# Optimization experiments

Measured on AMD Instinct MI355X. Metric: run time of the kernel, lower is better.

The kernel has to match this reference:

```python
import jax, jax.numpy as jnp
import numpy as np
from jax import lax

B, T, H, L, NV = 2048, 100, 256, 128, 5  # batch, max_len, hidden, latent, len(NUC_VOCAB)


def setup_inputs() -> dict:
    key = jax.random.key(0)
    ks = jax.random.split(key, 13)
    s = 0.05
    inp = {
        "x_seq": jax.random.uniform(ks[0], (B, T, NV), dtype=jnp.float32),
        "hidden_states": jax.random.normal(ks[1], (B, H), dtype=jnp.float32) * 0.1,
        "tree_latent_vec": jax.random.normal(ks[2], (B, L), dtype=jnp.float32),
        "graph_latent_vec": jax.random.normal(ks[3], (B, L), dtype=jnp.float32),
        "lengths": jnp.maximum(1, jax.random.randint(ks[4], (B,), 0, T + 1)).astype(jnp.int32),
        # concat_squash_linear: (H + L) -> H
        "W_cs": jax.random.normal(ks[5], (H + L, H), dtype=jnp.float32) * s,
        "b_cs": jnp.zeros((H,), dtype=jnp.float32),
        # GRU cell linears: (H + NV) -> H, acting on cat([x, h])
        "W_z": jax.random.normal(ks[6], (NV + H, H), dtype=jnp.float32) * s,
        "b_z": jnp.zeros((H,), dtype=jnp.float32),
        "W_r": jax.random.normal(ks[7], (NV + H, H), dtype=jnp.float32) * s,
        "b_r": jnp.zeros((H,), dtype=jnp.float32),
        "W_h": jax.random.normal(ks[8], (NV + H, H), dtype=jnp.float32) * s,
        "b_h": jnp.zeros((H,), dtype=jnp.float32),
    }
    return inp


def _decode(x_seq, hidden_states, tree_latent_vec, graph_latent_vec, lengths,
            W_cs, b_cs, W_z, b_z, W_r, b_r, W_h, b_h):
    # concat volatile hidden state with graph latent, squash back to H
    h0 = jax.nn.relu(jnp.concatenate([hidden_states, graph_latent_vec], axis=-1) @ W_cs + b_cs)

    def gru_step(h, x):  # h: [B,H], x: [B,NV]
        xh = jnp.concatenate([x, h], axis=-1)          # [B, NV+H]
        z = jax.nn.sigmoid(xh @ W_z + b_z)
        r = jax.nn.sigmoid(xh @ W_r + b_r)
        xg = jnp.concatenate([x, r * h], axis=-1)
        pre_h = jnp.tanh(xg @ W_h + b_h)
        new_h = (1.0 - z) * h + z * pre_h
        return new_h, new_h

    _, hs = lax.scan(gru_step, h0, jnp.swapaxes(x_seq, 0, 1))  # [T,B,H]
    all_h = jnp.swapaxes(hs, 0, 1)                              # [B,T,H]

    # gather hidden state at last valid timestep (pre_padding_idx)
    new_h = jnp.take_along_axis(all_h, (lengths - 1)[:, None, None], axis=1)[:, 0]  # [B,H]

    # per-segment max-pool over valid positions (segment_representation)
    mask = jnp.arange(T)[None, :] < lengths[:, None]            # [B,T]
    seg_rep = jnp.max(jnp.where(mask[:, :, None], all_h, -jnp.inf), axis=1)  # [B,H]

    # depadded token features concatenated with per-batch tree/graph latents;
    # kept padded [B,T,.] with zeros at invalid positions (fixed-shape form)
    tok = jnp.concatenate([
        all_h,
        jnp.broadcast_to(tree_latent_vec[:, None, :], (B, T, L)),
        jnp.broadcast_to(graph_latent_vec[:, None, :], (B, T, L)),
    ], axis=-1)                                                 # [B,T,H+2L]
    all_hidden_states = jnp.where(mask[:, :, None], tok, 0.0)
    return new_h, all_hidden_states, seg_rep


def reference(x_seq, hidden_states, tree_latent_vec, graph_latent_vec, lengths,
              W_cs, b_cs, W_z, b_z, W_r, b_r, W_h, b_h):
    return _decode(x_seq, hidden_states, tree_latent_vec, graph_latent_vec, lengths,
                   W_cs, b_cs, W_z, b_z, W_r, b_r, W_h, b_h)
```

## Files before the change

### kernel.cpp

```cpp
#include <hip/hip_runtime.h>
#include <stdint.h>

#define B_N 2048
#define T_N 100
#define H_N 256
#define L_N 128
#define NV_N 5
#define COLS 512

#define KCS 384
#define RB 8

#define KT_N 9
#define PZ_STR 260
#define HB_STR 296

#define NKQ 2
#define KQH 128
#define CH 16
#define NCH 8
#define HSTR 264

static constexpr int OUT_ALLH = B_N * H_N;
static constexpr int OUT_SEG  = OUT_ALLH + B_N * T_N * COLS;

typedef __attribute__((ext_vector_type(8))) short bf16x8v;
typedef __attribute__((ext_vector_type(4))) float f32x4v;

__device__ __align__(16) uint16_t g_frag[3 * KT_N * 16 * 64 * 8];

__device__ __forceinline__ float bits2f(uint32_t u) {
    union { uint32_t u; float f; } v; v.u = u; return v.f;
}
__device__ __forceinline__ uint16_t f2bf(float f) {
    union { float f; uint32_t u; } v; v.f = f;
    uint32_t r = (v.u + 0x7FFFu + ((v.u >> 16) & 1u)) >> 16;
    return (uint16_t)r;
}

__device__ __forceinline__ int detect_f32(const uint32_t* __restrict__ w) {
    int cnt = 0;
    #pragma unroll 8
    for (int i = 0; i < 64; ++i) {
        uint32_t e = (w[i] >> 23) & 0xFFu;
        cnt += (e >= 97u && e <= 130u) ? 1 : 0;
    }
    return cnt >= 32 ? 1 : 0;
}

__device__ __forceinline__ float bld1(const void* p, int idx) {
    return bits2f(((uint32_t)((const uint16_t*)p)[idx]) << 16);
}
__device__ __forceinline__ void bld4(const void* p, int idx, float f[4]) {
    uint2 u = *(const uint2*)((const uint16_t*)p + idx);
    f[0] = bits2f(u.x << 16); f[1] = bits2f(u.x & 0xFFFF0000u);
    f[2] = bits2f(u.y << 16); f[3] = bits2f(u.y & 0xFFFF0000u);
}
__device__ __forceinline__ void bst4(void* p, int idx, const float f[4]) {
    uint2 u;
    u.x = (uint32_t)f2bf(f[0]) | ((uint32_t)f2bf(f[1]) << 16);
    u.y = (uint32_t)f2bf(f[2]) | ((uint32_t)f2bf(f[3]) << 16);
    *(uint2*)((uint16_t*)p + idx) = u;
}
__device__ __forceinline__ void bst4z(void* p, int idx) {
    *(uint2*)((uint16_t*)p + idx) = make_uint2(0u, 0u);
}

template <bool F32> struct IO;
template <> struct IO<true> {
    using Raw2 = float2;
    static __device__ __forceinline__ Raw2 ldraw2(const void* p, int idx) {
        return *(const float2*)((const float*)p + idx);
    }
    static __device__ __forceinline__ void cvt2(const Raw2& u, float f[2]) { f[0] = u.x; f[1] = u.y; }
    static __device__ __forceinline__ void ld4(const void* p, int idx, float f[4]) {
        const float4 v = *(const float4*)((const float*)p + idx);
        f[0] = v.x; f[1] = v.y; f[2] = v.z; f[3] = v.w;
    }
    static __device__ __forceinline__ float ld1(const void* p, int idx) { return ((const float*)p)[idx]; }
    static __device__ __forceinline__ void st4(void* p, int idx, const float f[4]) {
        *(float4*)((float*)p + idx) = make_float4(f[0], f[1], f[2], f[3]);
    }
    static __device__ __forceinline__ void st4z(void* p, int idx) {
        *(float4*)((float*)p + idx) = make_float4(0.f, 0.f, 0.f, 0.f);
    }
};
template <> struct IO<false> {
    using Raw2 = uint32_t;
    static __device__ __forceinline__ Raw2 ldraw2(const void* p, int idx) {
        return *(const uint32_t*)((const uint16_t*)p + idx);
    }
    static __device__ __forceinline__ void cvt2(const Raw2& u, float f[2]) {
        f[0] = bits2f(u << 16); f[1] = bits2f(u & 0xFFFF0000u);
    }
    static __device__ __forceinline__ void ld4(const void* p, int idx, float f[4]) { bld4(p, idx, f); }
    static __device__ __forceinline__ float ld1(const void* p, int idx) { return bld1(p, idx); }
    static __device__ __forceinline__ void st4(void* p, int idx, const float f[4]) { bst4(p, idx, f); }
    static __device__ __forceinline__ void st4z(void* p, int idx) { bst4z(p, idx); }
};

__device__ __forceinline__ float sigmoid_f(float x) {
    x = fminf(fmaxf(x, -30.f), 30.f);
    return 1.f / (1.f + __expf(-x));
}
__device__ __forceinline__ float tanh_f(float x) {
    x = fminf(fmaxf(x, -15.f), 15.f);
    float e = __expf(-2.f * x);
    return (1.f - e) / (1.f + e);
}

template <bool F32>
__global__ __launch_bounds__(256) void latent_fill_kernel(
    const void* __restrict__ tree,
    const void* __restrict__ graph,
    const int* __restrict__ lengths,
    const void* __restrict__ Wcs_detect,
    void* __restrict__ out)
{
    __shared__ int s_is32;
    if (threadIdx.x == 0) s_is32 = detect_f32((const uint32_t*)Wcs_detect);
    __syncthreads();
    if ((s_is32 != 0) != F32) return;

    int idx = (int)(blockIdx.x * 256 + threadIdx.x);
    int c = (idx & 31) * 8;
    int bt = idx >> 5;
    int t = bt % T_N;
    int b = bt / T_N;

    int dst = OUT_ALLH + bt * COLS + H_N + c;
    if (t < lengths[b]) {
        float v[8];
        if (c < L_N) {
            IO<F32>::ld4(tree, b * L_N + c, v);
            IO<F32>::ld4(tree, b * L_N + c + 4, v + 4);
        } else {
            IO<F32>::ld4(graph, b * L_N + (c - L_N), v);
            IO<F32>::ld4(graph, b * L_N + (c - L_N) + 4, v + 4);
        }
        IO<F32>::st4(out, dst, v);
        IO<F32>::st4(out, dst + 4, v + 4);
    } else {
        IO<F32>::st4z(out, dst);
        IO<F32>::st4z(out, dst + 4);
    }
}

__global__ __launch_bounds__(256) void prep_kernel(
    const void* __restrict__ Wz, const void* __restrict__ Wr,
    const void* __restrict__ Wh, const void* __restrict__ Wcs_detect)
{
    __shared__ int s_is32;
    if (threadIdx.x == 0) s_is32 = detect_f32((const uint32_t*)Wcs_detect);
    __syncthreads();
    const int is32 = s_is32;

    int g = (int)(blockIdx.x * 256 + threadIdx.x);
    int lane  = g & 63;
    int rest  = g >> 6;
    int nt    = rest & 15;
    int rest2 = rest >> 4;
    int kt    = rest2 % KT_N;
    int mat   = rest2 / KT_N;
    if (mat > 2) return;

    const void* W = (mat == 0) ? Wz : (mat == 1) ? Wr : Wh;
    const int n = nt * 16 + (lane & 15);
    uint16_t u[8];
    #pragma unroll
    for (int j = 0; j < 8; ++j) {
        int k = kt * 32 + ((lane >> 4) * 8) + j;
        int srow = (k < 256) ? (k + NV_N) : ((k <= 260) ? (k - 256) : -1);
        uint16_t v = 0;
        if (srow >= 0) {
            if (is32) v = f2bf(((const float*)W)[srow * H_N + n]);
            else      v = ((const uint16_t*)W)[srow * H_N + n];
        }
        u[j] = v;
    }
    uint4 o;
    o.x = (uint32_t)u[0] | ((uint32_t)u[1] << 16);
    o.y = (uint32_t)u[2] | ((uint32_t)u[3] << 16);
    o.z = (uint32_t)u[4] | ((uint32_t)u[5] << 16);
    o.w = (uint32_t)u[6] | ((uint32_t)u[7] << 16);
    *(uint4*)((char*)g_frag + (size_t)g * 16) = o;
}

__global__ __launch_bounds__(256, 1) void gru_mfma(
    const void* __restrict__ x_seq,
    const void* __restrict__ hidden,
    const void* __restrict__ graph,
    const int* __restrict__ lengths,
    const void* __restrict__ Wcs, const void* __restrict__ bcs,
    const void* __restrict__ bz,  const void* __restrict__ br,
    const void* __restrict__ bh,  void* __restrict__ out)
{
    __shared__ float PzS[16 * PZ_STR];
    __shared__ float PrS[16 * PZ_STR];
    __shared__ uint16_t hbf[16 * HB_STR];
    __shared__ uint16_t gbf[16 * HB_STR];
    __shared__ int s_is32;
    __shared__ int s_len[RB];

    if (threadIdx.x == 0) s_is32 = detect_f32((const uint32_t*)Wcs);
    __syncthreads();
    if (s_is32 != 0) return;

    const int tid  = threadIdx.x;
    const int lane = tid & 63;
    const int wv   = tid >> 6;
    const int ntb  = wv * 4;
    const int ro   = tid >> 5;
    const int c0g  = (tid & 31) * 8;

    if (tid < RB) {
        int L = lengths[blockIdx.x * RB + tid];
        s_len[tid] = min(max(L, 1), T_N);
    }
    for (int i = tid; i < 16 * HB_STR; i += 256) { hbf[i] = 0; gbf[i] = 0; }
    __syncthreads();

    const int b0  = blockIdx.x * RB;
    const int bo  = b0 + ro;
    const int len = s_len[ro];
    int maxlen = 1;
    #pragma unroll
    for (int i = 0; i < RB; ++i) maxlen = max(maxlen, s_len[i]);

    {
        float* cs = PzS;
        for (int i = tid; i < RB * KCS; i += 256) {
            int r = i / KCS, k = i - r * KCS;
            int bb = b0 + r;
            float v = (k < H_N) ? bld1(hidden, bb * H_N + k)
                                : bld1(graph,  bb * L_N + (k - H_N));
            cs[r * 388 + k] = v;
        }
    }
    __syncthreads();

    float h[8];
    {
        const float* cs = PzS;
        float acc[8];
        bld4(bcs, c0g, acc); bld4(bcs, c0g + 4, acc + 4);
        for (int k = 0; k < KCS; k += 4) {
            const float4 hv = *(const float4*)&cs[ro * 388 + k];
            const float hvv[4] = {hv.x, hv.y, hv.z, hv.w};
            #pragma unroll
            for (int kk = 0; kk < 4; ++kk) {
                float w[8];
                bld4(Wcs, (k + kk) * H_N + c0g, w);
                bld4(Wcs, (k + kk) * H_N + c0g + 4, w + 4);
                #pragma unroll
                for (int j = 0; j < 8; ++j) acc[j] += hvv[kk] * w[j];
            }
        }
        #pragma unroll
        for (int j = 0; j < 8; ++j) h[j] = fmaxf(acc[j], 0.f);
    }

    float bzv[8], brv[8], bhv[8];
    bld4(bz, c0g, bzv); bld4(bz, c0g + 4, bzv + 4);
    bld4(br, c0g, brv); bld4(br, c0g + 4, brv + 4);
    bld4(bh, c0g, bhv); bld4(bh, c0g + 4, bhv + 4);

    float smax[8];
    #pragma unroll
    for (int j = 0; j < 8; ++j) smax[j] = -1e30f;

    __syncthreads();

#define STORE_HILO(BUF, VALS) { \
    union { bf16x8v v; uint16_t u[8]; } hi_, lo_; \
    _Pragma("unroll") \
    for (int j_ = 0; j_ < 8; ++j_) { \
        uint16_t a_ = f2bf(VALS[j_]); \
        hi_.u[j_] = a_; \
        lo_.u[j_] = f2bf(VALS[j_] - bits2f((uint32_t)a_ << 16)); \
    } \
    *(bf16x8v*)&BUF[ro * HB_STR + c0g] = hi_.v; \
    *(bf16x8v*)&BUF[(8 + ro) * HB_STR + c0g] = lo_.v; }

    STORE_HILO(hbf, h)
    const int xr = tid / NV_N;
    const int xi = tid - xr * NV_N;
    float xv = 0.f;
    if (tid < RB * NV_N) {
        float x0 = bld1(x_seq, ((b0 + xr) * T_N + 0) * NV_N + xi);
        uint16_t xh = f2bf(x0);
        uint16_t xl = f2bf(x0 - bits2f((uint32_t)xh << 16));
        hbf[xr * HB_STR + 256 + xi] = xh; hbf[(8 + xr) * HB_STR + 256 + xi] = xl;
        gbf[xr * HB_STR + 256 + xi] = xh; gbf[(8 + xr) * HB_STR + 256 + xi] = xl;
        xv = bld1(x_seq, ((b0 + xr) * T_N + 1) * NV_N + xi);
    }
    __syncthreads();

    const bf16x8v* wsW = (const bf16x8v*)g_frag;
    float z[8];

#define LDB1(KT, S) { \
    _Pragma("unroll") \
    for (int nt_ = 0; nt_ < 4; ++nt_) { \
        Bz[S][nt_] = wsW[((0 * KT_N + (KT)) * 16 + ntb + nt_) * 64 + lane]; \
        Br[S][nt_] = wsW[((1 * KT_N + (KT)) * 16 + ntb + nt_) * 64 + lane]; \
    } }
#define MMA1(KT, S) { \
    bf16x8v a_ = *(const bf16x8v*)&hbf[(lane & 15) * HB_STR + (KT) * 32 + ((lane >> 4) * 8)]; \
    _Pragma("unroll") \
    for (int nt_ = 0; nt_ < 4; ++nt_) { \
        accz[nt_] = __builtin_amdgcn_mfma_f32_16x16x32_bf16(a_, Bz[S][nt_], accz[nt_], 0, 0, 0); \
        accr[nt_] = __builtin_amdgcn_mfma_f32_16x16x32_bf16(a_, Br[S][nt_], accr[nt_], 0, 0, 0); \
    } }
#define LDB2(KT, S) { \
    _Pragma("unroll") \
    for (int nt_ = 0; nt_ < 4; ++nt_) \
        Bh[S][nt_] = wsW[((2 * KT_N + (KT)) * 16 + ntb + nt_) * 64 + lane]; }
#define MMA2(KT, S) { \
    bf16x8v a_ = *(const bf16x8v*)&gbf[(lane & 15) * HB_STR + (KT) * 32 + ((lane >> 4) * 8)]; \
    _Pragma("unroll") \
    for (int nt_ = 0; nt_ < 4; ++nt_) \
        acch[nt_] = __builtin_amdgcn_mfma_f32_16x16x32_bf16(a_, Bh[S][nt_], acch[nt_], 0, 0, 0); }

    #pragma unroll 1
    for (int t = 0; t < maxlen; ++t) {
        {
            bf16x8v Bz[3][4], Br[3][4];
            f32x4v accz[4], accr[4];
            #pragma unroll
            for (int nt_ = 0; nt_ < 4; ++nt_) {
                accz[nt_] = {0.f, 0.f, 0.f, 0.f};
                accr[nt_] = {0.f, 0.f, 0.f, 0.f};
            }
            LDB1(0, 0) LDB1(1, 1) LDB1(2, 2)
            MMA1(0, 0) LDB1(3, 0)
            MMA1(1, 1) LDB1(4, 1)
            MMA1(2, 2) LDB1(5, 2)
            MMA1(3, 0) LDB1(6, 0)
            MMA1(4, 1) LDB1(7, 1)
            MMA1(5, 2) LDB1(8, 2)
            MMA1(6, 0) MMA1(7, 1) MMA1(8, 2)
            #pragma unroll
            for (int nt_ = 0; nt_ < 4; ++nt_) {
                #pragma unroll
                for (int i_ = 0; i_ < 4; ++i_) {
                    const int m_ = (lane >> 4) * 4 + i_;
                    const int cc = (ntb + nt_) * 16 + (lane & 15);
                    PzS[m_ * PZ_STR + cc] = accz[nt_][i_];
                    PrS[m_ * PZ_STR + cc] = accr[nt_][i_];
                }
            }
        }
        __syncthreads();

        {
            const float4 za = *(const float4*)&PzS[ro * PZ_STR + c0g];
            const float4 zb = *(const float4*)&PzS[ro * PZ_STR + c0g + 4];
            const float4 zc = *(const float4*)&PzS[(8 + ro) * PZ_STR + c0g];
            const float4 zd = *(const float4*)&PzS[(8 + ro) * PZ_STR + c0g + 4];
            const float4 ra = *(const float4*)&PrS[ro * PZ_STR + c0g];
            const float4 rb = *(const float4*)&PrS[ro * PZ_STR + c0g + 4];
            const float4 rc = *(const float4*)&PrS[(8 + ro) * PZ_STR + c0g];
            const float4 rd = *(const float4*)&PrS[(8 + ro) * PZ_STR + c0g + 4];
            float sz[8] = {bzv[0] + za.x + zc.x, bzv[1] + za.y + zc.y,
                           bzv[2] + za.z + zc.z, bzv[3] + za.w + zc.w,
                           bzv[4] + zb.x + zd.x, bzv[5] + zb.y + zd.y,
                           bzv[6] + zb.z + zd.z, bzv[7] + zb.w + zd.w};
            float sr[8] = {brv[0] + ra.x + rc.x, brv[1] + ra.y + rc.y,
                           brv[2] + ra.z + rc.z, brv[3] + ra.w + rc.w,
                           brv[4] + rb.x + rd.x, brv[5] + rb.y + rd.y,
                           brv[6] + rb.z + rd.z, brv[7] + rb.w + rd.w};
            float rh[8];
            #pragma unroll
            for (int j = 0; j < 8; ++j) {
                z[j]  = sigmoid_f(sz[j]);
                rh[j] = sigmoid_f(sr[j]) * h[j];
            }
            STORE_HILO(gbf, rh)
        }
        __syncthreads();

        {
            bf16x8v Bh[3][4];
            f32x4v acch[4];
            #pragma unroll
            for (int nt_ = 0; nt_ < 4; ++nt_) acch[nt_] = {0.f, 0.f, 0.f, 0.f};
            LDB2(0, 0) LDB2(1, 1) LDB2(2, 2)
            MMA2(0, 0) LDB2(3, 0)
            MMA2(1, 1) LDB2(4, 1)
            MMA2(2, 2) LDB2(5, 2)
            MMA2(3, 0) LDB2(6, 0)
            MMA2(4, 1) LDB2(7, 1)
            MMA2(5, 2) LDB2(8, 2)
            MMA2(6, 0) MMA2(7, 1) MMA2(8, 2)
            #pragma unroll
            for (int nt_ = 0; nt_ < 4; ++nt_) {
                #pragma unroll
                for (int i_ = 0; i_ < 4; ++i_) {
                    const int m_ = (lane >> 4) * 4 + i_;
                    PzS[m_ * PZ_STR + (ntb + nt_) * 16 + (lane & 15)] = acch[nt_][i_];
                }
            }
        }
        __syncthreads();

        {
            const float4 ga = *(const float4*)&PzS[ro * PZ_STR + c0g];
            const float4 gb = *(const float4*)&PzS[ro * PZ_STR + c0g + 4];
            const float4 gc = *(const float4*)&PzS[(8 + ro) * PZ_STR + c0g];
            const float4 gd = *(const float4*)&PzS[(8 + ro) * PZ_STR + c0g + 4];
            float sg[8] = {bhv[0] + ga.x + gc.x, bhv[1] + ga.y + gc.y,
                           bhv[2] + ga.z + gc.z, bhv[3] + ga.w + gc.w,
                           bhv[4] + gb.x + gd.x, bhv[5] + gb.y + gd.y,
                           bhv[6] + gb.z + gd.z, bhv[7] + gb.w + gd.w};
            const bool active = (t < len);
            float hs[8];
            #pragma unroll
            for (int j = 0; j < 8; ++j) {
                float pre = tanh_f(sg[j]);
                float hn  = (1.f - z[j]) * h[j] + z[j] * pre;
                hn = active ? hn : h[j];
                h[j]  = hn;
                hs[j] = active ? hn : 0.f;
                smax[j] = active ? fmaxf(smax[j], hn) : smax[j];
            }
            const int ob = OUT_ALLH + (bo * T_N + t) * COLS + c0g;
            bst4(out, ob, hs);
            bst4(out, ob + 4, hs + 4);
            if (t == len - 1) {
                bst4(out, bo * H_N + c0g, h);
                bst4(out, bo * H_N + c0g + 4, h + 4);
            }
            STORE_HILO(hbf, h)
        }
        if (tid < RB * NV_N) {
            uint16_t xh = f2bf(xv);
            uint16_t xl = f2bf(xv - bits2f((uint32_t)xh << 16));
            hbf[xr * HB_STR + 256 + xi] = xh; hbf[(8 + xr) * HB_STR + 256 + xi] = xl;
            gbf[xr * HB_STR + 256 + xi] = xh; gbf[(8 + xr) * HB_STR + 256 + xi] = xl;
            int tn = (t + 2 < T_N) ? (t + 2) : (T_N - 1);
            xv = bld1(x_seq, ((b0 + xr) * T_N + tn) * NV_N + xi);
        }
        __syncthreads();
    }

#undef LDB1
#undef MMA1
#undef LDB2
#undef MMA2
#undef STORE_HILO

    for (int t = maxlen; t < T_N; ++t) {
        const int ob = OUT_ALLH + (bo * T_N + t) * COLS + c0g;
        bst4z(out, ob);
        bst4z(out, ob + 4);
    }
    bst4(out, OUT_SEG + bo * H_N + c0g, smax);
    bst4(out, OUT_SEG + bo * H_N + c0g + 4, smax + 4);
}

template <bool F32>
__global__ __launch_bounds__(256, 1) void gru_kernel(
    const void* __restrict__ x_seq,
    const void* __restrict__ hidden,
    const void* __restrict__ graph,
    const int* __restrict__ lengths,
    const void* __restrict__ Wcs, const void* __restrict__ bcs,
    const void* __restrict__ Wz,  const void* __restrict__ bz,
    const void* __restrict__ Wr,  const void* __restrict__ br,
    const void* __restrict__ Wh,  const void* __restrict__ bh,
    void* __restrict__ out)
{
    __shared__ float Pz[NKQ][RB][H_N];
    __shared__ float Pr[NKQ][RB][H_N];
    __shared__ float hstage[RB][HSTR];
    __shared__ float gstage[RB][HSTR];
    __shared__ int s_is32;
    __shared__ int s_len[RB];

    if (threadIdx.x == 0) s_is32 = detect_f32((const uint32_t*)Wcs);
    __syncthreads();
    if ((s_is32 != 0) != F32) return;

    const int tid = threadIdx.x;
    const int kq  = tid >> 7;
    const int c0  = (tid & 127) * 2;
    const int ro  = tid >> 5;
    const int c0g = (tid & 31) * 8;
    const int kh0 = kq * KQH;

    if (tid < RB) {
        int L = lengths[blockIdx.x * RB + tid];
        s_len[tid] = min(max(L, 1), T_N);
    }
    __syncthreads();

    const int b0  = blockIdx.x * RB;
    const int bo  = b0 + ro;
    const int len = s_len[ro];
    int maxlen = 1;
    #pragma unroll
    for (int i = 0; i < RB; ++i) maxlen = max(maxlen, s_len[i]);

    {
        float* cs = &Pz[0][0][0];
        for (int i = tid; i < RB * KCS; i += 256) {
            int r = i / KCS;
            int k = i - r * KCS;
            int bb = b0 + r;
            float v = (k < H_N) ? IO<F32>::ld1(hidden, bb * H_N + k)
                                : IO<F32>::ld1(graph,  bb * L_N + (k - H_N));
            cs[r * 388 + k] = v;
        }
    }
    __syncthreads();

    float h[8];
    {
        const float* cs = &Pz[0][0][0];
        float acc[8];
        IO<F32>::ld4(bcs, c0g, acc);
        IO<F32>::ld4(bcs, c0g + 4, acc + 4);
        for (int k = 0; k < KCS; k += 4) {
            const float4 hv = *reinterpret_cast<const float4*>(&cs[ro * 388 + k]);
            const float hvv[4] = {hv.x, hv.y, hv.z, hv.w};
            #pragma unroll
            for (int kk = 0; kk < 4; ++kk) {
                float w[8];
                IO<F32>::ld4(Wcs, (k + kk) * H_N + c0g, w);
                IO<F32>::ld4(Wcs, (k + kk) * H_N + c0g + 4, w + 4);
                #pragma unroll
                for (int j = 0; j < 8; ++j) acc[j] += hvv[kk] * w[j];
            }
        }
        #pragma unroll
        for (int j = 0; j < 8; ++j) h[j] = fmaxf(acc[j], 0.f);
    }

    float bzv[8], brv[8], bhv[8];
    IO<F32>::ld4(bz, c0g, bzv); IO<F32>::ld4(bz, c0g + 4, bzv + 4);
    IO<F32>::ld4(br, c0g, brv); IO<F32>::ld4(br, c0g + 4, brv + 4);
    IO<F32>::ld4(bh, c0g, bhv); IO<F32>::ld4(bh, c0g + 4, bhv + 4);

    float smax[8];
    #pragma unroll
    for (int j = 0; j < 8; ++j) smax[j] = -1e30f;

    __syncthreads();

    *reinterpret_cast<float4*>(&hstage[ro][c0g])     = make_float4(h[0], h[1], h[2], h[3]);
    *reinterpret_cast<float4*>(&hstage[ro][c0g + 4]) = make_float4(h[4], h[5], h[6], h[7]);

    const int xr = tid / NV_N;
    const int xi = tid - xr * NV_N;
    float xv = 0.f;
    if (tid < RB * NV_N) {
        float x0 = IO<F32>::ld1(x_seq, ((b0 + xr) * T_N + 0) * NV_N + xi);
        hstage[xr][H_N + xi] = x0;
        gstage[xr][H_N + xi] = x0;
        int tn = (1 < T_N) ? 1 : 0;
        xv = IO<F32>::ld1(x_seq, ((b0 + xr) * T_N + tn) * NV_N + xi);
    }
    __syncthreads();

    float z[8];
    typename IO<F32>::Raw2 zA[CH], rA[CH], zB[CH], rB[CH], hA[CH], hB[CH];
    typename IO<F32>::Raw2 xzb[NV_N], xrb[NV_N], xhb[NV_N];

#define P1_ISSUE(CHN, RZ, RR) { \
    const int kb_ = 5 + kh0 + (CHN) * CH; \
    _Pragma("unroll") \
    for (int i_ = 0; i_ < CH; ++i_) { \
        RZ[i_] = IO<F32>::ldraw2(Wz, (kb_ + i_) * H_N + c0); \
        RR[i_] = IO<F32>::ldraw2(Wr, (kb_ + i_) * H_N + c0); \
    } \
    __builtin_amdgcn_sched_barrier(0); }
#define P1_CONSUME(CHN, RZ, RR) { \
    const int kb_ = kh0 + (CHN) * CH; \
    _Pragma("unroll") \
    for (int g_ = 0; g_ < CH / 2; ++g_) { \
        float2 hr_[RB]; \
        _Pragma("unroll") \
        for (int r_ = 0; r_ < RB; ++r_) \
            hr_[r_] = *reinterpret_cast<const float2*>(&hstage[r_][kb_ + 2 * g_]); \
        _Pragma("unroll") \
        for (int u_ = 0; u_ < 2; ++u_) { \
            float wz2_[2], wr2_[2]; \
            IO<F32>::cvt2(RZ[2 * g_ + u_], wz2_); \
            IO<F32>::cvt2(RR[2 * g_ + u_], wr2_); \
            _Pragma("unroll") \
            for (int r_ = 0; r_ < RB; ++r_) { \
                const float hv_ = u_ ? hr_[r_].y : hr_[r_].x; \
                az[r_][0] += hv_ * wz2_[0]; \
                az[r_][1] += hv_ * wz2_[1]; \
                ar[r_][0] += hv_ * wr2_[0]; \
                ar[r_][1] += hv_ * wr2_[1]; \
            } } } }
#define P2_ISSUE(CHN, RH) { \
    const int kb_ = 5 + kh0 + (CHN) * CH; \
    _Pragma("unroll") \
    for (int i_ = 0; i_ < CH; ++i_) \
        RH[i_] = IO<F32>::ldraw2(Wh, (kb_ + i_) * H_N + c0); \
    __builtin_amdgcn_sched_barrier(0); }
#define P2_CONSUME(CHN, RH) { \
    const int kb_ = kh0 + (CHN) * CH; \
    _Pragma("unroll") \
    for (int g_ = 0; g_ < CH / 2; ++g_) { \
        float2 gr_[RB]; \
        _Pragma("unroll") \
        for (int r_ = 0; r_ < RB; ++r_) \
            gr_[r_] = *reinterpret_cast<const float2*>(&gstage[r_][kb_ + 2 * g_]); \
        _Pragma("unroll") \
        for (int u_ = 0; u_ < 2; ++u_) { \
            float wh2_[2]; \
            IO<F32>::cvt2(RH[2 * g_ + u_], wh2_); \
            _Pragma("unroll") \
            for (int r_ = 0; r_ < RB; ++r_) { \
                const float gv_ = u_ ? gr_[r_].y : gr_[r_].x; \
                ag[r_][0] += gv_ * wh2_[0]; \
                ag[r_][1] += gv_ * wh2_[1]; \
            } } } }
#define PX_ISSUE() if (kq == 0) { \
    _Pragma("unroll") \
    for (int i_ = 0; i_ < NV_N; ++i_) { \
        xzb[i_] = IO<F32>::ldraw2(Wz, i_ * H_N + c0); \
        xrb[i_] = IO<F32>::ldraw2(Wr, i_ * H_N + c0); \
    } }
#define PXH_ISSUE() if (kq == 0) { \
    _Pragma("unroll") \
    for (int i_ = 0; i_ < NV_N; ++i_) \
        xhb[i_] = IO<F32>::ldraw2(Wh, i_ * H_N + c0); }
#define P1X_CONSUME() if (kq == 0) { \
    _Pragma("unroll") \
    for (int i_ = 0; i_ < NV_N; ++i_) { \
        float wz2_[2], wr2_[2]; \
        IO<F32>::cvt2(xzb[i_], wz2_); \
        IO<F32>::cvt2(xrb[i_], wr2_); \
        _Pragma("unroll") \
        for (int r_ = 0; r_ < RB; ++r_) { \
            const float xv_ = hstage[r_][H_N + i_]; \
            az[r_][0] += xv_ * wz2_[0]; \
            az[r_][1] += xv_ * wz2_[1]; \
            ar[r_][0] += xv_ * wr2_[0]; \
            ar[r_][1] += xv_ * wr2_[1]; \
        } } }
#define P2X_CONSUME() if (kq == 0) { \
    _Pragma("unroll") \
    for (int i_ = 0; i_ < NV_N; ++i_) { \
        float wh2_[2]; \
        IO<F32>::cvt2(xhb[i_], wh2_); \
        _Pragma("unroll") \
        for (int r_ = 0; r_ < RB; ++r_) { \
            const float xv_ = gstage[r_][H_N + i_]; \
            ag[r_][0] += xv_ * wh2_[0]; \
            ag[r_][1] += xv_ * wh2_[1]; \
        } } }

    PX_ISSUE();
    P1_ISSUE(0, zA, rA);

    #pragma unroll 1
    for (int t = 0; t < maxlen; ++t) {
        float az[RB][2], ar[RB][2];
        #pragma unroll
        for (int r = 0; r < RB; ++r) {
            az[r][0] = 0.f; az[r][1] = 0.f;
            ar[r][0] = 0.f; ar[r][1] = 0.f;
        }
        #pragma unroll 1
        for (int ch = 0; ch < NCH; ch += 2) {
            P1_ISSUE(ch + 1, zB, rB);
            P1_CONSUME(ch, zA, rA);
            if (ch + 2 < NCH) { P1_ISSUE(ch + 2, zA, rA); }
            else              { P2_ISSUE(0, hA); PXH_ISSUE(); }
            P1_CONSUME(ch + 1, zB, rB);
        }
        P1X_CONSUME();
        #pragma unroll
        for (int r = 0; r < RB; ++r) {
            *reinterpret_cast<float2*>(&Pz[kq][r][c0]) = make_float2(az[r][0], az[r][1]);
            *reinterpret_cast<float2*>(&Pr[kq][r][c0]) = make_float2(ar[r][0], ar[r][1]);
        }
        __syncthreads();

        {
            float sz[8], sr[8];
            #pragma unroll
            for (int j = 0; j < 8; ++j) { sz[j] = bzv[j]; sr[j] = brv[j]; }
            #pragma unroll
            for (int q = 0; q < NKQ; ++q) {
                float4 a = *reinterpret_cast<const float4*>(&Pz[q][ro][c0g]);
                float4 b = *reinterpret_cast<const float4*>(&Pz[q][ro][c0g + 4]);
                sz[0] += a.x; sz[1] += a.y; sz[2] += a.z; sz[3] += a.w;
                sz[4] += b.x; sz[5] += b.y; sz[6] += b.z; sz[7] += b.w;
                a = *reinterpret_cast<const float4*>(&Pr[q][ro][c0g]);
                b = *reinterpret_cast<const float4*>(&Pr[q][ro][c0g + 4]);
                sr[0] += a.x; sr[1] += a.y; sr[2] += a.z; sr[3] += a.w;
                sr[4] += b.x; sr[5] += b.y; sr[6] += b.z; sr[7] += b.w;
            }
            float rh[8];
            #pragma unroll
            for (int j = 0; j < 8; ++j) {
                z[j] = sigmoid_f(sz[j]);
                rh[j] = sigmoid_f(sr[j]) * h[j];
            }
            *reinterpret_cast<float4*>(&gstage[ro][c0g])     = make_float4(rh[0], rh[1], rh[2], rh[3]);
            *reinterpret_cast<float4*>(&gstage[ro][c0g + 4]) = make_float4(rh[4], rh[5], rh[6], rh[7]);
        }
        __syncthreads();

        float ag[RB][2];
        #pragma unroll
        for (int r = 0; r < RB; ++r) { ag[r][0] = 0.f; ag[r][1] = 0.f; }
        #pragma unroll 1
        for (int ch = 0; ch < NCH; ch += 2) {
            P2_ISSUE(ch + 1, hB);
            P2_CONSUME(ch, hA);
            if (ch + 2 < NCH) { P2_ISSUE(ch + 2, hA); }
            else              { P1_ISSUE(0, zA, rA); PX_ISSUE(); }
            P2_CONSUME(ch + 1, hB);
        }
        P2X_CONSUME();
        #pragma unroll
        for (int r = 0; r < RB; ++r)
            *reinterpret_cast<float2*>(&Pz[kq][r][c0]) = make_float2(ag[r][0], ag[r][1]);
        __syncthreads();

        {
            float sg[8];
            #pragma unroll
            for (int j = 0; j < 8; ++j) sg[j] = bhv[j];
            #pragma unroll
            for (int q = 0; q < NKQ; ++q) {
                float4 a = *reinterpret_cast<const float4*>(&Pz[q][ro][c0g]);
                float4 b = *reinterpret_cast<const float4*>(&Pz[q][ro][c0g + 4]);
                sg[0] += a.x; sg[1] += a.y; sg[2] += a.z; sg[3] += a.w;
                sg[4] += b.x; sg[5] += b.y; sg[6] += b.z; sg[7] += b.w;
            }
            const bool active = (t < len);
            float hs[8];
            #pragma unroll
            for (int j = 0; j < 8; ++j) {
                float pre = tanh_f(sg[j]);
                float hn  = (1.f - z[j]) * h[j] + z[j] * pre;
                hn = active ? hn : h[j];
                h[j]  = hn;
                hs[j] = active ? hn : 0.f;
                smax[j] = active ? fmaxf(smax[j], hn) : smax[j];
            }
            const int ob = OUT_ALLH + (bo * T_N + t) * COLS + c0g;
            IO<F32>::st4(out, ob, hs);
            IO<F32>::st4(out, ob + 4, hs + 4);
            if (t == len - 1) {
                IO<F32>::st4(out, bo * H_N + c0g, h);
                IO<F32>::st4(out, bo * H_N + c0g + 4, h + 4);
            }
            *reinterpret_cast<float4*>(&hstage[ro][c0g])     = make_float4(h[0], h[1], h[2], h[3]);
            *reinterpret_cast<float4*>(&hstage[ro][c0g + 4]) = make_float4(h[4], h[5], h[6], h[7]);
        }
        if (tid < RB * NV_N) {
            hstage[xr][H_N + xi] = xv;
            gstage[xr][H_N + xi] = xv;
            int tn = (t + 2 < T_N) ? (t + 2) : (T_N - 1);
            xv = IO<F32>::ld1(x_seq, ((b0 + xr) * T_N + tn) * NV_N + xi);
        }
        __syncthreads();
    }

#undef P1_ISSUE
#undef P1_CONSUME
#undef P2_ISSUE
#undef P2_CONSUME
#undef PX_ISSUE
#undef PXH_ISSUE
#undef P1X_CONSUME
#undef P2X_CONSUME

    for (int t = maxlen; t < T_N; ++t) {
        const int ob = OUT_ALLH + (bo * T_N + t) * COLS + c0g;
        IO<F32>::st4z(out, ob);
        IO<F32>::st4z(out, ob + 4);
    }
    IO<F32>::st4(out, OUT_SEG + bo * H_N + c0g, smax);
    IO<F32>::st4(out, OUT_SEG + bo * H_N + c0g + 4, smax + 4);
}

extern "C" void kernel_launch(void* const* d_in, const int* in_sizes, int n_in,
                              void* d_out, int out_size, void* d_ws, size_t ws_size,
                              hipStream_t stream) {
    const void* x_seq  = d_in[0];
    const void* hidden = d_in[1];
    const void* tree   = d_in[2];
    const void* graph  = d_in[3];
    const int*  lens   = (const int*)d_in[4];
    const void* Wcs    = d_in[5];
    const void* bcs    = d_in[6];
    const void* Wz     = d_in[7];
    const void* bz     = d_in[8];
    const void* Wr     = d_in[9];
    const void* br     = d_in[10];
    const void* Wh     = d_in[11];
    const void* bh     = d_in[12];
    void* out = d_out;
    (void)d_ws; (void)ws_size;

    long long work = (long long)B_N * T_N * 32;
    int fill_blocks = (int)(work / 256);

    hipLaunchKernelGGL((latent_fill_kernel<true>),  dim3(fill_blocks), dim3(256), 0, stream,
                       tree, graph, lens, Wcs, out);
    hipLaunchKernelGGL((latent_fill_kernel<false>), dim3(fill_blocks), dim3(256), 0, stream,
                       tree, graph, lens, Wcs, out);

    hipLaunchKernelGGL(prep_kernel, dim3(108), dim3(256), 0, stream,
                       Wz, Wr, Wh, Wcs);
    hipLaunchKernelGGL(gru_mfma, dim3(B_N / RB), dim3(256), 0, stream,
                       x_seq, hidden, graph, lens,
                       Wcs, bcs, bz, br, bh, out);
    hipLaunchKernelGGL((gru_kernel<true>), dim3(B_N / RB), dim3(256), 0, stream,
                       x_seq, hidden, graph, lens,
                       Wcs, bcs, Wz, bz, Wr, br, Wh, bh, out);
}
```

Measured before the change: 4.094 ms.

## Route fp32 inputs through MFMA GRU kernel using split bf16 hi/lo weights

Enables the MFMA-based GRU kernel for fp32 inputs, which previously always ran the scalar fp32 kernel. The prep kernel now emits two bf16 weight fragments per matrix, a high part and a residual low part. The MFMA loop runs over the doubled K range so the recurrent matmuls get extra mantissa bits while using bf16 matrix cores. It also switches the loads and stores in that kernel to fp32, and changes the host to launch the bf16 scalar kernel variant, which does nothing for fp32 inputs. The cost is twice the MFMA work and fragment traffic, plus some precision risk versus true fp32 because of the truncated split products.

```diff
diff --git a/kernel.cpp b/kernel.cpp
--- a/kernel.cpp
+++ b/kernel.cpp
@@ -11,7 +11,8 @@
 #define KCS 384
 #define RB 8
 
-#define KT_N 9
+#define KT_N 18
+#define KHALF 9
 #define PZ_STR 260
 #define HB_STR 296
 
@@ -66,6 +67,20 @@
     *(uint2*)((uint16_t*)p + idx) = make_uint2(0u, 0u);
 }
 
+__device__ __forceinline__ float fld1(const void* p, int idx) {
+    return ((const float*)p)[idx];
+}
+__device__ __forceinline__ void fld4(const void* p, int idx, float f[4]) {
+    const float4 v = *(const float4*)((const float*)p + idx);
+    f[0] = v.x; f[1] = v.y; f[2] = v.z; f[3] = v.w;
+}
+__device__ __forceinline__ void fst4(void* p, int idx, const float f[4]) {
+    *(float4*)((float*)p + idx) = make_float4(f[0], f[1], f[2], f[3]);
+}
+__device__ __forceinline__ void fst4z(void* p, int idx) {
+    *(float4*)((float*)p + idx) = make_float4(0.f, 0.f, 0.f, 0.f);
+}
+
 template <bool F32> struct IO;
 template <> struct IO<true> {
     using Raw2 = float2;
@@ -73,17 +88,10 @@
         return *(const float2*)((const float*)p + idx);
     }
     static __device__ __forceinline__ void cvt2(const Raw2& u, float f[2]) { f[0] = u.x; f[1] = u.y; }
-    static __device__ __forceinline__ void ld4(const void* p, int idx, float f[4]) {
-        const float4 v = *(const float4*)((const float*)p + idx);
-        f[0] = v.x; f[1] = v.y; f[2] = v.z; f[3] = v.w;
-    }
-    static __device__ __forceinline__ float ld1(const void* p, int idx) { return ((const float*)p)[idx]; }
-    static __device__ __forceinline__ void st4(void* p, int idx, const float f[4]) {
-        *(float4*)((float*)p + idx) = make_float4(f[0], f[1], f[2], f[3]);
-    }
-    static __device__ __forceinline__ void st4z(void* p, int idx) {
-        *(float4*)((float*)p + idx) = make_float4(0.f, 0.f, 0.f, 0.f);
-    }
+    static __device__ __forceinline__ void ld4(const void* p, int idx, float f[4]) { fld4(p, idx, f); }
+    static __device__ __forceinline__ float ld1(const void* p, int idx) { return fld1(p, idx); }
+    static __device__ __forceinline__ void st4(void* p, int idx, const float f[4]) { fst4(p, idx, f); }
+    static __device__ __forceinline__ void st4z(void* p, int idx) { fst4z(p, idx); }
 };
 template <> struct IO<false> {
     using Raw2 = uint32_t;
@@ -169,12 +177,15 @@
     uint16_t u[8];
     #pragma unroll
     for (int j = 0; j < 8; ++j) {
-        int k = kt * 32 + ((lane >> 4) * 8) + j;
+        int k = (kt % KHALF) * 32 + ((lane >> 4) * 8) + j;
         int srow = (k < 256) ? (k + NV_N) : ((k <= 260) ? (k - 256) : -1);
         uint16_t v = 0;
         if (srow >= 0) {
-            if (is32) v = f2bf(((const float*)W)[srow * H_N + n]);
-            else      v = ((const uint16_t*)W)[srow * H_N + n];
+            float w = is32 ? ((const float*)W)[srow * H_N + n]
+                           : bld1(W, srow * H_N + n);
+            uint16_t hi = f2bf(w);
+            if (kt < KHALF) v = hi;
+            else            v = f2bf(w - bits2f((uint32_t)hi << 16));
         }
         u[j] = v;
     }
@@ -204,7 +215,7 @@
 
     if (threadIdx.x == 0) s_is32 = detect_f32((const uint32_t*)Wcs);
     __syncthreads();
-    if (s_is32 != 0) return;
+    if (s_is32 == 0) return;
 
     const int tid  = threadIdx.x;
     const int lane = tid & 63;
@@ -232,8 +243,8 @@
         for (int i = tid; i < RB * KCS; i += 256) {
             int r = i / KCS, k = i - r * KCS;
             int bb = b0 + r;
-            float v = (k < H_N) ? bld1(hidden, bb * H_N + k)
-                                : bld1(graph,  bb * L_N + (k - H_N));
+            float v = (k < H_N) ? fld1(hidden, bb * H_N + k)
+                                : fld1(graph,  bb * L_N + (k - H_N));
             cs[r * 388 + k] = v;
         }
     }
@@ -243,15 +254,15 @@
     {
         const float* cs = PzS;
         float acc[8];
-        bld4(bcs, c0g, acc); bld4(bcs, c0g + 4, acc + 4);
+        fld4(bcs, c0g, acc); fld4(bcs, c0g + 4, acc + 4);
         for (int k = 0; k < KCS; k += 4) {
             const float4 hv = *(const float4*)&cs[ro * 388 + k];
             const float hvv[4] = {hv.x, hv.y, hv.z, hv.w};
             #pragma unroll
             for (int kk = 0; kk < 4; ++kk) {
                 float w[8];
-                bld4(Wcs, (k + kk) * H_N + c0g, w);
-                bld4(Wcs, (k + kk) * H_N + c0g + 4, w + 4);
+                fld4(Wcs, (k + kk) * H_N + c0g, w);
+                fld4(Wcs, (k + kk) * H_N + c0g + 4, w + 4);
                 #pragma unroll
                 for (int j = 0; j < 8; ++j) acc[j] += hvv[kk] * w[j];
             }
@@ -261,9 +272,9 @@
     }
 
     float bzv[8], brv[8], bhv[8];
-    bld4(bz, c0g, bzv); bld4(bz, c0g + 4, bzv + 4);
-    bld4(br, c0g, brv); bld4(br, c0g + 4, brv + 4);
-    bld4(bh, c0g, bhv); bld4(bh, c0g + 4, bhv + 4);
+    fld4(bz, c0g, bzv); fld4(bz, c0g + 4, bzv + 4);
+    fld4(br, c0g, brv); fld4(br, c0g + 4, brv + 4);
+    fld4(bh, c0g, bhv); fld4(bh, c0g + 4, bhv + 4);
 
     float smax[8];
     #pragma unroll
@@ -287,12 +298,12 @@
     const int xi = tid - xr * NV_N;
     float xv = 0.f;
     if (tid < RB * NV_N) {
-        float x0 = bld1(x_seq, ((b0 + xr) * T_N + 0) * NV_N + xi);
+        float x0 = fld1(x_seq, ((b0 + xr) * T_N + 0) * NV_N + xi);
         uint16_t xh = f2bf(x0);
         uint16_t xl = f2bf(x0 - bits2f((uint32_t)xh << 16));
         hbf[xr * HB_STR + 256 + xi] = xh; hbf[(8 + xr) * HB_STR + 256 + xi] = xl;
         gbf[xr * HB_STR + 256 + xi] = xh; gbf[(8 + xr) * HB_STR + 256 + xi] = xl;
-        xv = bld1(x_seq, ((b0 + xr) * T_N + 1) * NV_N + xi);
+        xv = fld1(x_seq, ((b0 + xr) * T_N + 1) * NV_N + xi);
     }
     __syncthreads();
 
@@ -306,7 +317,7 @@
         Br[S][nt_] = wsW[((1 * KT_N + (KT)) * 16 + ntb + nt_) * 64 + lane]; \
     } }
 #define MMA1(KT, S) { \
-    bf16x8v a_ = *(const bf16x8v*)&hbf[(lane & 15) * HB_STR + (KT) * 32 + ((lane >> 4) * 8)]; \
+    bf16x8v a_ = *(const bf16x8v*)&hbf[(lane & 15) * HB_STR + ((KT) % KHALF) * 32 + ((lane >> 4) * 8)]; \
     _Pragma("unroll") \
     for (int nt_ = 0; nt_ < 4; ++nt_) { \
         accz[nt_] = __builtin_amdgcn_mfma_f32_16x16x32_bf16(a_, Bz[S][nt_], accz[nt_], 0, 0, 0); \
@@ -317,7 +328,7 @@
     for (int nt_ = 0; nt_ < 4; ++nt_) \
         Bh[S][nt_] = wsW[((2 * KT_N + (KT)) * 16 + ntb + nt_) * 64 + lane]; }
 #define MMA2(KT, S) { \
-    bf16x8v a_ = *(const bf16x8v*)&gbf[(lane & 15) * HB_STR + (KT) * 32 + ((lane >> 4) * 8)]; \
+    bf16x8v a_ = *(const bf16x8v*)&gbf[(lane & 15) * HB_STR + ((KT) % KHALF) * 32 + ((lane >> 4) * 8)]; \
     _Pragma("unroll") \
     for (int nt_ = 0; nt_ < 4; ++nt_) \
         acch[nt_] = __builtin_amdgcn_mfma_f32_16x16x32_bf16(a_, Bh[S][nt_], acch[nt_], 0, 0, 0); }
@@ -333,13 +344,22 @@
                 accr[nt_] = {0.f, 0.f, 0.f, 0.f};
             }
             LDB1(0, 0) LDB1(1, 1) LDB1(2, 2)
-            MMA1(0, 0) LDB1(3, 0)
-            MMA1(1, 1) LDB1(4, 1)
-            MMA1(2, 2) LDB1(5, 2)
-            MMA1(3, 0) LDB1(6, 0)
-            MMA1(4, 1) LDB1(7, 1)
-            MMA1(5, 2) LDB1(8, 2)
-            MMA1(6, 0) MMA1(7, 1) MMA1(8, 2)
+            MMA1(0, 0)  LDB1(3, 0)
+            MMA1(1, 1)  LDB1(4, 1)
+            MMA1(2, 2)  LDB1(5, 2)
+            MMA1(3, 0)  LDB1(6, 0)
+            MMA1(4, 1)  LDB1(7, 1)
+            MMA1(5, 2)  LDB1(8, 2)
+            MMA1(6, 0)  LDB1(9, 0)
+            MMA1(7, 1)  LDB1(10, 1)
+            MMA1(8, 2)  LDB1(11, 2)
+            MMA1(9, 0)  LDB1(12, 0)
+            MMA1(10, 1) LDB1(13, 1)
+            MMA1(11, 2) LDB1(14, 2)
+            MMA1(12, 0) LDB1(15, 0)
+            MMA1(13, 1) LDB1(16, 1)
+            MMA1(14, 2) LDB1(17, 2)
+            MMA1(15, 0) MMA1(16, 1) MMA1(17, 2)
             #pragma unroll
             for (int nt_ = 0; nt_ < 4; ++nt_) {
                 #pragma unroll
@@ -386,13 +406,22 @@
             #pragma unroll
             for (int nt_ = 0; nt_ < 4; ++nt_) acch[nt_] = {0.f, 0.f, 0.f, 0.f};
             LDB2(0, 0) LDB2(1, 1) LDB2(2, 2)
-            MMA2(0, 0) LDB2(3, 0)
-            MMA2(1, 1) LDB2(4, 1)
-            MMA2(2, 2) LDB2(5, 2)
-            MMA2(3, 0) LDB2(6, 0)
-            MMA2(4, 1) LDB2(7, 1)
-            MMA2(5, 2) LDB2(8, 2)
-            MMA2(6, 0) MMA2(7, 1) MMA2(8, 2)
+            MMA2(0, 0)  LDB2(3, 0)
+            MMA2(1, 1)  LDB2(4, 1)
+            MMA2(2, 2)  LDB2(5, 2)
+            MMA2(3, 0)  LDB2(6, 0)
+            MMA2(4, 1)  LDB2(7, 1)
+            MMA2(5, 2)  LDB2(8, 2)
+            MMA2(6, 0)  LDB2(9, 0)
+            MMA2(7, 1)  LDB2(10, 1)
+            MMA2(8, 2)  LDB2(11, 2)
+            MMA2(9, 0)  LDB2(12, 0)
+            MMA2(10, 1) LDB2(13, 1)
+            MMA2(11, 2) LDB2(14, 2)
+            MMA2(12, 0) LDB2(15, 0)
+            MMA2(13, 1) LDB2(16, 1)
+            MMA2(14, 2) LDB2(17, 2)
+            MMA2(15, 0) MMA2(16, 1) MMA2(17, 2)
             #pragma unroll
             for (int nt_ = 0; nt_ < 4; ++nt_) {
                 #pragma unroll
@@ -425,11 +454,11 @@
                 smax[j] = active ? fmaxf(smax[j], hn) : smax[j];
             }
             const int ob = OUT_ALLH + (bo * T_N + t) * COLS + c0g;
-            bst4(out, ob, hs);
-            bst4(out, ob + 4, hs + 4);
+            fst4(out, ob, hs);
+            fst4(out, ob + 4, hs + 4);
             if (t == len - 1) {
-                bst4(out, bo * H_N + c0g, h);
-                bst4(out, bo * H_N + c0g + 4, h + 4);
+                fst4(out, bo * H_N + c0g, h);
+                fst4(out, bo * H_N + c0g + 4, h + 4);
             }
             STORE_HILO(hbf, h)
         }
@@ -439,7 +468,7 @@
             hbf[xr * HB_STR + 256 + xi] = xh; hbf[(8 + xr) * HB_STR + 256 + xi] = xl;
             gbf[xr * HB_STR + 256 + xi] = xh; gbf[(8 + xr) * HB_STR + 256 + xi] = xl;
             int tn = (t + 2 < T_N) ? (t + 2) : (T_N - 1);
-            xv = bld1(x_seq, ((b0 + xr) * T_N + tn) * NV_N + xi);
+            xv = fld1(x_seq, ((b0 + xr) * T_N + tn) * NV_N + xi);
         }
         __syncthreads();
     }
@@ -452,11 +481,11 @@
 
     for (int t = maxlen; t < T_N; ++t) {
         const int ob = OUT_ALLH + (bo * T_N + t) * COLS + c0g;
-        bst4z(out, ob);
-        bst4z(out, ob + 4);
-    }
-    bst4(out, OUT_SEG + bo * H_N + c0g, smax);
-    bst4(out, OUT_SEG + bo * H_N + c0g + 4, smax + 4);
+        fst4z(out, ob);
+        fst4z(out, ob + 4);
+    }
+    fst4(out, OUT_SEG + bo * H_N + c0g, smax);
+    fst4(out, OUT_SEG + bo * H_N + c0g + 4, smax + 4);
 }
 
 template <bool F32>
@@ -812,12 +841,12 @@
     hipLaunchKernelGGL((latent_fill_kernel<false>), dim3(fill_blocks), dim3(256), 0, stream,
                        tree, graph, lens, Wcs, out);
 
-    hipLaunchKernelGGL(prep_kernel, dim3(108), dim3(256), 0, stream,
+    hipLaunchKernelGGL(prep_kernel, dim3(216), dim3(256), 0, stream,
                        Wz, Wr, Wh, Wcs);
     hipLaunchKernelGGL(gru_mfma, dim3(B_N / RB), dim3(256), 0, stream,
                        x_seq, hidden, graph, lens,
                        Wcs, bcs, bz, br, bh, out);
-    hipLaunchKernelGGL((gru_kernel<true>), dim3(B_N / RB), dim3(256), 0, stream,
+    hipLaunchKernelGGL((gru_kernel<false>), dim3(B_N / RB), dim3(256), 0, stream,
                        x_seq, hidden, graph, lens,
                        Wcs, bcs, Wz, bz, Wr, br, Wh, bh, out);
 }
```

After: 5.020 ms. +22.6%, slower.
